# Kernel optimization log

Measured on AMD Instinct MI355X. Metric: run time of the kernel, lower is better.

Reference implementation:

```python
import jax, jax.numpy as jnp
import numpy as np

TOPK, NUM_CLASSES, ALPHA, BETA, EPS = 13, 80, 1.0, 6.0, 1e-9


def setup_inputs() -> dict:
    key = jax.random.key(0)
    ks = jax.random.split(key, 8)
    bs, na, nmax, nc = 16, 33600, 64, 80
    img = 1280.0
    pd_scores = jax.random.uniform(ks[0], (bs, na, nc), dtype=jnp.float32)
    p_xy = jax.random.uniform(ks[1], (bs, na, 2), dtype=jnp.float32) * img
    p_r = jax.random.uniform(ks[2], (bs, na, 1), dtype=jnp.float32) * 60.0 + 5.0
    pd_circles = jnp.concatenate([p_xy, p_r], axis=-1)
    anc_points = jax.random.uniform(ks[3], (na, 2), dtype=jnp.float32) * img
    gt_labels = jax.random.randint(ks[4], (bs, nmax, 1), 0, nc, dtype=jnp.int32)
    g_xy = jax.random.uniform(ks[5], (bs, nmax, 2), dtype=jnp.float32) * img
    g_r = jax.random.uniform(ks[6], (bs, nmax, 1), dtype=jnp.float32) * 100.0 + 10.0
    gt_bboxes = jnp.concatenate([g_xy, g_r], axis=-1)
    mask_gt = (jax.random.uniform(ks[7], (bs, nmax, 1)) < 0.7).astype(jnp.float32)
    return {"pd_scores": pd_scores, "pd_circles": pd_circles, "anc_points": anc_points,
            "gt_labels": gt_labels, "gt_bboxes": gt_bboxes, "mask_gt": mask_gt}


def _assign(pd_scores, pd_circles, anc_points, gt_labels, gt_bboxes, mask_gt):
    bs, na, nc = pd_scores.shape
    nmax = gt_bboxes.shape[1]
    dt = pd_scores.dtype
    gxy, gr = gt_bboxes[..., :2], gt_bboxes[..., 2]            # (bs,nmax,2),(bs,nmax)
    # --- select_candidates_in_gts: anchor center within gt circle ---
    diff = gxy[:, :, None, :] - anc_points[None, None, :, :]    # (bs,nmax,na,2)
    dist_anc = jnp.linalg.norm(diff, axis=-1)                   # (bs,nmax,na)
    mask_in_gts = (dist_anc <= gr[..., None]).astype(dt)
    valid = (mask_in_gts * mask_gt) > 0                         # (bs,nmax,na) bool
    # --- get_box_metrics ---
    labels = gt_labels[..., 0].astype(jnp.int32)                # (bs,nmax)
    b_idx = jnp.arange(bs)[:, None]
    bbox_scores = pd_scores[b_idx, :, labels]                   # (bs,nmax,na)
    bbox_scores = jnp.where(valid, bbox_scores, 0.0)
    d = jnp.sqrt((gxy[..., 0][:, :, None] - pd_circles[..., 0][:, None, :]) ** 2
                 + (gxy[..., 1][:, :, None] - pd_circles[..., 1][:, None, :]) ** 2)
    rsum = gr[..., None] + pd_circles[..., 2][:, None, :]
    iou = jnp.maximum((rsum - d) / rsum, 0.0)
    overlaps = jnp.where(valid, iou, 0.0)
    align_metric = bbox_scores ** ALPHA * overlaps ** BETA      # (bs,nmax,na)
    # --- select_topk_candidates ---
    topk_metrics, topk_idxs = jax.lax.top_k(align_metric, TOPK)  # (bs,nmax,TOPK)
    topk_mask = (jnp.max(topk_metrics, axis=-1, keepdims=True) > EPS)
    ones = jnp.broadcast_to(topk_mask, topk_idxs.shape).astype(dt)
    counts = jnp.zeros((bs, nmax, na), dtype=dt).at[
        jnp.arange(bs)[:, None, None], jnp.arange(nmax)[None, :, None], topk_idxs
    ].add(ones)
    mask_topk = jnp.where(counts > 1, 0.0, counts)
    mask_pos = mask_topk * mask_in_gts * mask_gt                # (bs,nmax,na)
    # --- select_highest_overlaps: resolve anchors claimed by multiple gts ---
    multi = jnp.sum(mask_pos, axis=-2, keepdims=True) > 1       # (bs,1,na)
    max_ov_idx = jnp.argmax(overlaps, axis=1)                   # (bs,na)
    is_max = (jnp.arange(nmax)[None, :, None] == max_ov_idx[:, None, :]).astype(dt)
    mask_pos = jnp.where(multi, is_max, mask_pos)
    fg_mask = jnp.sum(mask_pos, axis=-2)                        # (bs,na)
    target_gt_idx = jnp.argmax(mask_pos, axis=-2)               # (bs,na)
    # --- get_targets ---
    target_labels = jnp.take_along_axis(labels, target_gt_idx, axis=1)  # (bs,na)
    target_bboxes = jnp.take_along_axis(gt_bboxes, target_gt_idx[..., None], axis=1)  # (bs,na,3)
    target_labels = jnp.maximum(target_labels, 0)
    target_scores = jax.nn.one_hot(target_labels, nc, dtype=dt) * (fg_mask[..., None] > 0)
    # --- normalize align metric ---
    am = align_metric * mask_pos
    pos_align = jnp.max(am, axis=-1, keepdims=True)             # (bs,nmax,1)
    pos_over = jnp.max(overlaps * mask_pos, axis=-1, keepdims=True)
    norm_align = jnp.max(am * pos_over / (pos_align + EPS), axis=-2)[..., None]  # (bs,na,1)
    target_scores = target_scores * norm_align
    return target_labels, target_bboxes, target_scores, (fg_mask > 0), target_gt_idx


def reference(pd_scores, pd_circles, anc_points, gt_labels, gt_bboxes, mask_gt):
    return _assign(pd_scores, pd_circles, anc_points, gt_labels, gt_bboxes, mask_gt)
```

## Files before the change

kernel.cpp:

```cpp
#include <hip/hip_runtime.h>
#include <hip/hip_bf16.h>
#include <cstdint>

#define BS    16
#define NA    33600
#define NMAX  64
#define NC    80
#define TOPKN 13
#define SEG   16
#define SEGLEN (NA / SEG)
#define EPSF  1e-9f

#define O_LAB 0
#define O_BOX 537600
#define O_SCR 2150400
#define O_FG  45158400
#define O_GT  45696000


__global__ __launch_bounds__(64) void k_topk_seg(
    const float* __restrict__ pd_scores,
    const float* __restrict__ pd_circles,
    const float* __restrict__ anc,
    const int*   __restrict__ gt_labels,
    const float* __restrict__ gt_bboxes,
    const float* __restrict__ mask_gt,
    float*       __restrict__ s1val,
    int*         __restrict__ s1idx)
{
    const int blk  = blockIdx.x;
    const int row  = blk >> 4;
    const int seg  = blk & (SEG - 1);
    const int lane = threadIdx.x;

    float* outv = s1val + (size_t)blk * TOPKN;
    int*   outi = s1idx + (size_t)blk * TOPKN;

    if (mask_gt[row] <= 0.f) {
        if (lane < TOPKN) { outv[lane] = -2.f; outi[lane] = 0x7fffffff; }
        return;
    }

    const float gx = gt_bboxes[row * 3 + 0];
    const float gy = gt_bboxes[row * 3 + 1];
    const float gr = gt_bboxes[row * 3 + 2];
    const int   lbl = gt_labels[row];
    const int   b   = row >> 6;
    const float* __restrict__ ps = pd_scores + (size_t)b * NA * NC + lbl;
    const float* __restrict__ pc = pd_circles + (size_t)b * NA * 3;
    const float2* __restrict__ anc2 = (const float2*)anc;

    float tv[TOPKN]; int ti[TOPKN];
#pragma unroll
    for (int k = 0; k < TOPKN; ++k) { tv[k] = -1.f; ti[k] = 0x7fffffff; }

    const int base = seg * SEGLEN;
    for (int a = base + lane; a < base + SEGLEN; a += 64) {
        float2 ap = anc2[a];
        float dx = gx - ap.x, dy = gy - ap.y;
        float m = 0.f;
        if (sqrtf(dx * dx + dy * dy) <= gr) {
            float px = pc[a * 3 + 0], py = pc[a * 3 + 1], pr = pc[a * 3 + 2];
            float ddx = gx - px, ddy = gy - py;
            float d  = sqrtf(ddx * ddx + ddy * ddy);
            float rs = gr + pr;
            float iou = fmaxf((rs - d) / rs, 0.f);
            float i2 = iou * iou;
            m = ps[(size_t)a * NC] * (i2 * i2 * i2);
        }
        if (m > tv[TOPKN - 1]) {
#pragma unroll
            for (int p = TOPKN - 1; p > 0; --p) {
                if (tv[p] < m) {
                    bool here = (tv[p - 1] >= m);
                    tv[p] = here ? m : tv[p - 1];
                    ti[p] = here ? a : ti[p - 1];
                }
            }
            if (tv[0] < m) { tv[0] = m; ti[0] = a; }
        }
    }

    float myv = -3.f; int myi = 0x7fffffff;
    for (int k = 0; k < TOPKN; ++k) {
        float v = tv[0]; int i = ti[0];
#pragma unroll
        for (int s = 1; s < 64; s <<= 1) {
            float vo = __shfl_xor(v, s);
            int   io = __shfl_xor(i, s);
            if (vo > v || (vo == v && io < i)) { v = vo; i = io; }
        }
        if (lane == k) { myv = v; myi = i; }
        bool own = (ti[0] == i);
#pragma unroll
        for (int p = 0; p < TOPKN - 1; ++p) {
            tv[p] = own ? tv[p + 1] : tv[p];
            ti[p] = own ? ti[p + 1] : ti[p];
        }
        if (own) { tv[TOPKN - 1] = -3.f; ti[TOPKN - 1] = 0x7fffffff; }
    }
    if (lane < TOPKN) { outv[lane] = myv; outi[lane] = myi; }
}

__global__ __launch_bounds__(64) void k_topk_merge(
    const float* __restrict__ s1val,
    const int*   __restrict__ s1idx,
    int*         __restrict__ topk_out)
{
    const int row  = blockIdx.x;
    const int lane = threadIdx.x;
    const float* __restrict__ v  = s1val + (size_t)row * SEG * TOPKN;
    const int*   __restrict__ ii = s1idx + (size_t)row * SEG * TOPKN;

    float sv[4]; int si[4];
#pragma unroll
    for (int q = 0; q < 4; ++q) {
        int c = lane + 64 * q;
        if (c < SEG * TOPKN) { sv[q] = v[c]; si[q] = ii[c]; }
        else                 { sv[q] = -3.f; si[q] = 0x7fffffff; }
    }

    float myv = -3.f; int myi = 0x7fffffff;
    for (int k = 0; k < TOPKN; ++k) {
        float bv = sv[0]; int bi = si[0];
#pragma unroll
        for (int q = 1; q < 4; ++q) {
            if (sv[q] > bv || (sv[q] == bv && si[q] < bi)) { bv = sv[q]; bi = si[q]; }
        }
#pragma unroll
        for (int s = 1; s < 64; s <<= 1) {
            float vo = __shfl_xor(bv, s);
            int   io = __shfl_xor(bi, s);
            if (vo > bv || (vo == bv && io < bi)) { bv = vo; bi = io; }
        }
        if (lane == k) { myv = bv; myi = bi; }
#pragma unroll
        for (int q = 0; q < 4; ++q) {
            if (si[q] == bi && sv[q] == bv) sv[q] = -3.f;
        }
    }
    float w0 = __shfl(myv, 0);
    if (lane < TOPKN)
        topk_out[row * TOPKN + lane] = (w0 > EPSF) ? myi : -1;
}

__global__ __launch_bounds__(256) void k_claims(
    const float* __restrict__ anc,
    const float* __restrict__ gt_bboxes,
    const int*   __restrict__ topk,
    int*         __restrict__ counts,
    int*         __restrict__ jsum)
{
    int t = blockIdx.x * 256 + threadIdx.x;
    if (t >= BS * NMAX * TOPKN) return;
    int r = t / TOPKN;
    int a = topk[t];
    if (a < 0) return;
    int b = r >> 6, j = r & 63;
    float gx = gt_bboxes[r * 3 + 0], gy = gt_bboxes[r * 3 + 1], gr = gt_bboxes[r * 3 + 2];
    float dx = gx - anc[a * 2 + 0], dy = gy - anc[a * 2 + 1];
    if (sqrtf(dx * dx + dy * dy) <= gr) {
        atomicAdd(counts + b * NA + a, 1);
        atomicAdd(jsum + b * NA + a, j);
    }
}

__global__ __launch_bounds__(256) void k_resolve(
    const float* __restrict__ pd_scores,
    const float* __restrict__ pd_circles,
    const float* __restrict__ anc,
    const int*   __restrict__ gt_labels,
    const float* __restrict__ gt_bboxes,
    const float* __restrict__ mask_gt,
    const int*   __restrict__ counts,
    const int*   __restrict__ jsum,
    int*         __restrict__ tgt_ws,
    float*       __restrict__ am_ws,
    unsigned*    __restrict__ pos_align,
    unsigned*    __restrict__ pos_over)
{
    int i = blockIdx.x * 256 + threadIdx.x;
    int b = i / NA, a = i - b * NA;
    int cnt = counts[i];
    float ax = anc[a * 2 + 0], ay = anc[a * 2 + 1];

    int tgt = -1;
    if (cnt == 1) {
        tgt = jsum[i];
    } else if (cnt > 1) {
        float px = pd_circles[((size_t)b * NA + a) * 3 + 0];
        float py = pd_circles[((size_t)b * NA + a) * 3 + 1];
        float pr = pd_circles[((size_t)b * NA + a) * 3 + 2];
        float best = -1.f; int bj = 0;
        for (int j = 0; j < NMAX; ++j) {
            int row = b * NMAX + j;
            float ov = 0.f;
            if (mask_gt[row] > 0.f) {
                float gx = gt_bboxes[row * 3 + 0], gy = gt_bboxes[row * 3 + 1], gr = gt_bboxes[row * 3 + 2];
                float dx = gx - ax, dy = gy - ay;
                if (sqrtf(dx * dx + dy * dy) <= gr) {
                    float ddx = gx - px, ddy = gy - py;
                    float d  = sqrtf(ddx * ddx + ddy * ddy);
                    float rs = gr + pr;
                    ov = fmaxf((rs - d) / rs, 0.f);
                }
            }
            if (ov > best) { best = ov; bj = j; }
        }
        tgt = bj;
    }
    tgt_ws[i] = tgt;

    float am = 0.f, ovv = 0.f;
    if (tgt >= 0) {
        int row = b * NMAX + tgt;
        if (mask_gt[row] > 0.f) {
            float gx = gt_bboxes[row * 3 + 0], gy = gt_bboxes[row * 3 + 1], gr = gt_bboxes[row * 3 + 2];
            float dx = gx - ax, dy = gy - ay;
            if (sqrtf(dx * dx + dy * dy) <= gr) {
                float px = pd_circles[((size_t)b * NA + a) * 3 + 0];
                float py = pd_circles[((size_t)b * NA + a) * 3 + 1];
                float pr = pd_circles[((size_t)b * NA + a) * 3 + 2];
                float ddx = gx - px, ddy = gy - py;
                float d  = sqrtf(ddx * ddx + ddy * ddy);
                float rs = gr + pr;
                float iou = fmaxf((rs - d) / rs, 0.f);
                float i2 = iou * iou;
                float s  = pd_scores[((size_t)b * NA + a) * NC + gt_labels[row]];
                am  = s * (i2 * i2 * i2);
                ovv = iou;
            }
        }
        atomicMax(pos_align + row, __float_as_uint(am));
        atomicMax(pos_over  + row, __float_as_uint(ovv));
    }
    am_ws[i] = am;
}

__global__ __launch_bounds__(256) void k_write(
    const int*      __restrict__ gt_labels,
    const float*    __restrict__ gt_bboxes,
    const int*      __restrict__ tgt_ws,
    const float*    __restrict__ am_ws,
    const unsigned* __restrict__ pos_align,
    const unsigned* __restrict__ pos_over,
    float*          __restrict__ out)
{
    int i = blockIdx.x * 256 + threadIdx.x;
    int b = i / NA;
    int tgt = tgt_ws[i];
    bool fg = (tgt >= 0);
    int jj  = fg ? tgt : 0;
    int row = b * NMAX + jj;

    int lbl = max(gt_labels[row], 0);
    out[O_LAB + i] = (float)lbl;
    out[O_BOX + (size_t)i * 3 + 0] = gt_bboxes[row * 3 + 0];
    out[O_BOX + (size_t)i * 3 + 1] = gt_bboxes[row * 3 + 1];
    out[O_BOX + (size_t)i * 3 + 2] = gt_bboxes[row * 3 + 2];
    out[O_FG + i] = fg ? 1.f : 0.f;
    out[O_GT + i] = (float)jj;

    if (fg) {
        float pa = __uint_as_float(pos_align[row]);
        float po = __uint_as_float(pos_over[row]);
        float norm = am_ws[i] * po / (pa + EPSF);
        out[O_SCR + (size_t)i * NC + lbl] = norm;
    }
}

extern "C" void kernel_launch(void* const* d_in, const int* in_sizes, int n_in,
                              void* d_out, int out_size, void* d_ws, size_t ws_size,
                              hipStream_t stream) {
    const float* pd_scores  = (const float*)d_in[0];
    const float* pd_circles = (const float*)d_in[1];
    const float* anc        = (const float*)d_in[2];
    const int*   gt_labels  = (const int*)d_in[3];
    const float* gt_bboxes  = (const float*)d_in[4];
    const float* mask_gt    = (const float*)d_in[5];
    float* out = (float*)d_out;

    char* ws = (char*)d_ws;
    int*      topk      = (int*)(ws + 0);
    float*    s1val     = (float*)(ws + 53248);
    int*      s1idx     = (int*)(ws + 905216);
    int*      counts    = (int*)(ws + 53248);
    int*      jsum      = (int*)(ws + 2203648);
    int*      tgt_ws    = (int*)(ws + 4354048);
    float*    am_ws     = (float*)(ws + 6504448);
    unsigned* pos_align = (unsigned*)(ws + 8654848);
    unsigned* pos_over  = (unsigned*)(ws + 8658944);

    hipMemsetAsync(out + O_SCR, 0, (size_t)BS * NA * NC * sizeof(float), stream);
    hipMemsetAsync(pos_align, 0, 2 * 1024 * sizeof(unsigned), stream);

    k_topk_seg<<<BS * NMAX * SEG, 64, 0, stream>>>(pd_scores, pd_circles, anc, gt_labels,
                                                   gt_bboxes, mask_gt, s1val, s1idx);
    k_topk_merge<<<BS * NMAX, 64, 0, stream>>>(s1val, s1idx, topk);

    hipMemsetAsync(counts, 0, 2 * 537600 * sizeof(int), stream);

    k_claims<<<(BS * NMAX * TOPKN + 255) / 256, 256, 0, stream>>>(anc, gt_bboxes, topk,
                                                                  counts, jsum);
    k_resolve<<<(BS * NA) / 256, 256, 0, stream>>>(pd_scores, pd_circles, anc, gt_labels,
                                                   gt_bboxes, mask_gt, counts, jsum,
                                                   tgt_ws, am_ws, pos_align, pos_over);
    k_write<<<(BS * NA) / 256, 256, 0, stream>>>(gt_labels, gt_bboxes, tgt_ws, am_ws,
                                                 pos_align, pos_over, out);
}
```

Before: 146.8 us.

## Fuse memsets into kernels, merge claim step, pack counts, write dense scores

Drops the three hipMemsetAsync calls. The topk segment kernel now zeroes the claim buffer and the pos_align/pos_over maxima, and the topk merge and claim kernels become one. Per-anchor count and gt-index sum are packed into a single 32-bit word, so one atomic replaces two. The score output is written densely with coalesced float4 stores that include the zeros, instead of a full memset followed by scattered single writes. Together these cut launches, the separate memset pass and atomic traffic, at the cost of relying on the packed low 20 bits never overflowing.

```diff
diff --git a/kernel.cpp b/kernel.cpp
--- a/kernel.cpp
+++ b/kernel.cpp
@@ -6,6 +6,7 @@
 #define NA    33600
 #define NMAX  64
 #define NC    80
+#define NQ    20
 #define TOPKN 13
 #define SEG   16
 #define SEGLEN (NA / SEG)
@@ -26,12 +27,24 @@
     const float* __restrict__ gt_bboxes,
     const float* __restrict__ mask_gt,
     float*       __restrict__ s1val,
-    int*         __restrict__ s1idx)
+    int*         __restrict__ s1idx,
+    unsigned*    __restrict__ pack,
+    unsigned*    __restrict__ pos_align,
+    unsigned*    __restrict__ pos_over)
 {
     const int blk  = blockIdx.x;
     const int row  = blk >> 4;
     const int seg  = blk & (SEG - 1);
     const int lane = threadIdx.x;
+
+    {
+        int gtid = blk * 64 + lane;
+        if (gtid < BS * NA) pack[gtid] = 0u;
+    }
+    if (seg == 0 && lane == 0) {
+        pos_align[row] = 0u;
+        pos_over[row]  = 0u;
+    }
 
     float* outv = s1val + (size_t)blk * TOPKN;
     int*   outi = s1idx + (size_t)blk * TOPKN;
@@ -102,10 +115,12 @@
     if (lane < TOPKN) { outv[lane] = myv; outi[lane] = myi; }
 }
 
-__global__ __launch_bounds__(64) void k_topk_merge(
+__global__ __launch_bounds__(64) void k_merge_claim(
     const float* __restrict__ s1val,
     const int*   __restrict__ s1idx,
-    int*         __restrict__ topk_out)
+    const float* __restrict__ anc,
+    const float* __restrict__ gt_bboxes,
+    unsigned*    __restrict__ pack)
 {
     const int row  = blockIdx.x;
     const int lane = threadIdx.x;
@@ -140,28 +155,16 @@
         }
     }
     float w0 = __shfl(myv, 0);
-    if (lane < TOPKN)
-        topk_out[row * TOPKN + lane] = (w0 > EPSF) ? myi : -1;
-}
-
-__global__ __launch_bounds__(256) void k_claims(
-    const float* __restrict__ anc,
-    const float* __restrict__ gt_bboxes,
-    const int*   __restrict__ topk,
-    int*         __restrict__ counts,
-    int*         __restrict__ jsum)
-{
-    int t = blockIdx.x * 256 + threadIdx.x;
-    if (t >= BS * NMAX * TOPKN) return;
-    int r = t / TOPKN;
-    int a = topk[t];
-    if (a < 0) return;
-    int b = r >> 6, j = r & 63;
-    float gx = gt_bboxes[r * 3 + 0], gy = gt_bboxes[r * 3 + 1], gr = gt_bboxes[r * 3 + 2];
-    float dx = gx - anc[a * 2 + 0], dy = gy - anc[a * 2 + 1];
-    if (sqrtf(dx * dx + dy * dy) <= gr) {
-        atomicAdd(counts + b * NA + a, 1);
-        atomicAdd(jsum + b * NA + a, j);
+    if (lane < TOPKN && w0 > EPSF) {
+        int a = myi;
+        float gx = gt_bboxes[row * 3 + 0];
+        float gy = gt_bboxes[row * 3 + 1];
+        float gr = gt_bboxes[row * 3 + 2];
+        float dx = gx - anc[a * 2 + 0], dy = gy - anc[a * 2 + 1];
+        if (sqrtf(dx * dx + dy * dy) <= gr) {
+            int b = row >> 6, j = row & 63;
+            atomicAdd(pack + b * NA + a, (1u << 20) | (unsigned)j);
+        }
     }
 }
 
@@ -172,8 +175,7 @@
     const int*   __restrict__ gt_labels,
     const float* __restrict__ gt_bboxes,
     const float* __restrict__ mask_gt,
-    const int*   __restrict__ counts,
-    const int*   __restrict__ jsum,
+    const unsigned* __restrict__ pack,
     int*         __restrict__ tgt_ws,
     float*       __restrict__ am_ws,
     unsigned*    __restrict__ pos_align,
@@ -181,12 +183,13 @@
 {
     int i = blockIdx.x * 256 + threadIdx.x;
     int b = i / NA, a = i - b * NA;
-    int cnt = counts[i];
+    unsigned p = pack[i];
+    int cnt = (int)(p >> 20);
     float ax = anc[a * 2 + 0], ay = anc[a * 2 + 1];
 
     int tgt = -1;
     if (cnt == 1) {
-        tgt = jsum[i];
+        tgt = (int)(p & 0xFFFFFu);
     } else if (cnt > 1) {
         float px = pd_circles[((size_t)b * NA + a) * 3 + 0];
         float py = pd_circles[((size_t)b * NA + a) * 3 + 1];
@@ -237,7 +240,7 @@
     am_ws[i] = am;
 }
 
-__global__ __launch_bounds__(256) void k_write(
+__global__ __launch_bounds__(256) void k_write_scores(
     const int*      __restrict__ gt_labels,
     const float*    __restrict__ gt_bboxes,
     const int*      __restrict__ tgt_ws,
@@ -246,8 +249,12 @@
     const unsigned* __restrict__ pos_over,
     float*          __restrict__ out)
 {
-    int i = blockIdx.x * 256 + threadIdx.x;
-    int b = i / NA;
+    __shared__ float s_n[256];
+    __shared__ int   s_l[256];
+
+    const int tid = threadIdx.x;
+    const int i = blockIdx.x * 256 + tid;
+    const int b = i / NA;
     int tgt = tgt_ws[i];
     bool fg = (tgt >= 0);
     int jj  = fg ? tgt : 0;
@@ -261,11 +268,29 @@
     out[O_FG + i] = fg ? 1.f : 0.f;
     out[O_GT + i] = (float)jj;
 
+    float nv = 0.f;
     if (fg) {
         float pa = __uint_as_float(pos_align[row]);
         float po = __uint_as_float(pos_over[row]);
-        float norm = am_ws[i] * po / (pa + EPSF);
-        out[O_SCR + (size_t)i * NC + lbl] = norm;
+        nv = am_ws[i] * po / (pa + EPSF);
+    }
+    s_n[tid] = nv;
+    s_l[tid] = lbl;
+    __syncthreads();
+
+    float4* __restrict__ scr = (float4*)(out + O_SCR) + (size_t)blockIdx.x * 256 * NQ;
+    for (int e = tid; e < 256 * NQ; e += 256) {
+        int il = e / NQ;
+        int q  = e - il * NQ;
+        float nvv = s_n[il];
+        int   lb  = s_l[il];
+        int   c0  = q * 4;
+        float4 vq; vq.x = 0.f; vq.y = 0.f; vq.z = 0.f; vq.w = 0.f;
+        if      (lb == c0)     vq.x = nvv;
+        else if (lb == c0 + 1) vq.y = nvv;
+        else if (lb == c0 + 2) vq.z = nvv;
+        else if (lb == c0 + 3) vq.w = nvv;
+        scr[e] = vq;
     }
 }
 
@@ -281,30 +306,21 @@
     float* out = (float*)d_out;
 
     char* ws = (char*)d_ws;
-    int*      topk      = (int*)(ws + 0);
-    float*    s1val     = (float*)(ws + 53248);
-    int*      s1idx     = (int*)(ws + 905216);
-    int*      counts    = (int*)(ws + 53248);
-    int*      jsum      = (int*)(ws + 2203648);
-    int*      tgt_ws    = (int*)(ws + 4354048);
-    float*    am_ws     = (float*)(ws + 6504448);
-    unsigned* pos_align = (unsigned*)(ws + 8654848);
-    unsigned* pos_over  = (unsigned*)(ws + 8658944);
-
-    hipMemsetAsync(out + O_SCR, 0, (size_t)BS * NA * NC * sizeof(float), stream);
-    hipMemsetAsync(pos_align, 0, 2 * 1024 * sizeof(unsigned), stream);
+    float*    s1val     = (float*)(ws + 0);
+    int*      s1idx     = (int*)(ws + 851968);
+    unsigned* pack      = (unsigned*)(ws + 1703936);
+    int*      tgt_ws    = (int*)(ws + 3854336);
+    float*    am_ws     = (float*)(ws + 6004736);
+    unsigned* pos_align = (unsigned*)(ws + 8155136);
+    unsigned* pos_over  = (unsigned*)(ws + 8159232);
 
     k_topk_seg<<<BS * NMAX * SEG, 64, 0, stream>>>(pd_scores, pd_circles, anc, gt_labels,
-                                                   gt_bboxes, mask_gt, s1val, s1idx);
-    k_topk_merge<<<BS * NMAX, 64, 0, stream>>>(s1val, s1idx, topk);
-
-    hipMemsetAsync(counts, 0, 2 * 537600 * sizeof(int), stream);
-
-    k_claims<<<(BS * NMAX * TOPKN + 255) / 256, 256, 0, stream>>>(anc, gt_bboxes, topk,
-                                                                  counts, jsum);
+                                                   gt_bboxes, mask_gt, s1val, s1idx,
+                                                   pack, pos_align, pos_over);
+    k_merge_claim<<<BS * NMAX, 64, 0, stream>>>(s1val, s1idx, anc, gt_bboxes, pack);
     k_resolve<<<(BS * NA) / 256, 256, 0, stream>>>(pd_scores, pd_circles, anc, gt_labels,
-                                                   gt_bboxes, mask_gt, counts, jsum,
+                                                   gt_bboxes, mask_gt, pack,
                                                    tgt_ws, am_ws, pos_align, pos_over);
-    k_write<<<(BS * NA) / 256, 256, 0, stream>>>(gt_labels, gt_bboxes, tgt_ws, am_ws,
-                                                 pos_align, pos_over, out);
-}
+    k_write_scores<<<(BS * NA) / 256, 256, 0, stream>>>(gt_labels, gt_bboxes, tgt_ws, am_ws,
+                                                        pos_align, pos_over, out);
+}
```

Measured after the change: 139.2 us. 5.2% less time.
